# Performance work log

Hardware: AMD Instinct MI355X
Metric: run time of the kernel (lower is better)

## Reference

```python
import jax, jax.numpy as jnp
import numpy as np

B, CIN, COUT, K, SDIM, H, W = 16, 512, 512, 3, 512, 64, 64


def setup_inputs() -> dict:
    key = jax.random.key(0)
    k1, k2, k3, k4 = jax.random.split(key, 4)
    return {
        "x": jax.random.normal(k1, (B, CIN, H, W), dtype=jnp.float32),
        "style": jax.random.normal(k2, (B, SDIM), dtype=jnp.float32),
        "weight": jax.random.normal(k3, (COUT, CIN, K, K), dtype=jnp.float32),
        "style_w": jax.random.normal(k4, (CIN, SDIM), dtype=jnp.float32),
        "style_b": jnp.ones((CIN,), dtype=jnp.float32),  # bias.data.fill_(1.0)
    }


def reference(x, style, weight, style_w, style_b):
    batch, in_ch, h, w_size = x.shape
    out_ch, _, ks, _ = weight.shape
    pad = ks // 2
    # EqualizedLinear: runtime weight scaling by 1/sqrt(fan_in)
    lin_scale = 1.0 / np.sqrt(style_w.shape[1])
    s = style @ (style_w * lin_scale).T + style_b  # [B, Cin]
    # modulate
    conv_scale = 1.0 / np.sqrt(in_ch * ks * ks)
    wmod = (weight[None] * conv_scale) * s[:, None, :, None, None]  # [B,Cout,Cin,k,k]
    # demodulate
    dcoef = jax.lax.rsqrt(jnp.sum(jnp.square(wmod), axis=(2, 3, 4)) + 1e-8)  # [B,Cout]
    wmod = wmod * dcoef[:, :, None, None, None]
    # grouped conv with groups = batch
    x_r = x.reshape(1, batch * in_ch, h, w_size)
    w_r = wmod.reshape(batch * out_ch, in_ch, ks, ks)
    out = jax.lax.conv_general_dilated(
        x_r, w_r,
        window_strides=(1, 1),
        padding=[(pad, pad), (pad, pad)],
        dimension_numbers=("NCHW", "OIHW", "NCHW"),
        feature_group_count=batch,
    )
    return out.reshape(batch, out_ch, h, w_size)
```

## Files before the change

### kernel.cpp

```cpp
#include <hip/hip_runtime.h>
#include <math.h>

#define B 16
#define CIN 512
#define COUT 512
#define SDIM 512
#define H 64
#define W 64

typedef short s16x8 __attribute__((ext_vector_type(8)));
typedef float f32x4 __attribute__((ext_vector_type(4)));
typedef float f32x16 __attribute__((ext_vector_type(16)));

__device__ __constant__ float LIN_SCALE  = 0.04419417382415922f;
__device__ __constant__ float CONV_SCALE = 0.014731391274719742f;

__device__ __forceinline__ ushort f2bf(float f) {
  unsigned u = __float_as_uint(f);
  return (ushort)((u + 0x7FFFu + ((u >> 16) & 1u)) >> 16);
}

#define GLOAD16(g, l)                                           \
  __builtin_amdgcn_global_load_lds(                             \
      (const __attribute__((address_space(1))) unsigned*)(g),   \
      (__attribute__((address_space(3))) unsigned*)(l), 16, 0, 0)

__global__ __launch_bounds__(256) void prep1_kernel(
    const float* __restrict__ w, const float* __restrict__ style,
    const float* __restrict__ style_w, const float* __restrict__ style_b,
    ushort* __restrict__ wt, float* __restrict__ wsq, float* __restrict__ s,
    float* __restrict__ s2) {
  const int tid = threadIdx.x;
  if (blockIdx.x < 128) {
    const int t = blockIdx.x * 256 + tid;
    const int so = t & 3;
    const int chunk = (t >> 2) & 15;
    const int co = t >> 6;
    const float4* wp =
        (const float4*)(w + ((size_t)co * 512 + chunk * 32 + so * 8) * 9);
    float wv[72];
#pragma unroll
    for (int i = 0; i < 18; ++i) {
      float4 v = wp[i];
      wv[4 * i + 0] = v.x; wv[4 * i + 1] = v.y;
      wv[4 * i + 2] = v.z; wv[4 * i + 3] = v.w;
    }
    {
      float q[8];
#pragma unroll
      for (int i = 0; i < 8; ++i) {
        float a = 0.f;
#pragma unroll
        for (int k = 0; k < 9; ++k) {
          float v = wv[i * 9 + k];
          a += v * v;
        }
        q[i] = a;
      }
      float4* qd = (float4*)(wsq + (size_t)co * 512 + chunk * 32 + so * 8);
      qd[0] = make_float4(q[0], q[1], q[2], q[3]);
      qd[1] = make_float4(q[4], q[5], q[6], q[7]);
    }
    const int cb = co >> 6, co64 = co & 63;
    ushort* dst = wt + (size_t)chunk * 147456 + (size_t)cb * 2048 +
                  (size_t)so * 512 + (size_t)co64 * 8;
#pragma unroll
    for (int j = 0; j < 9; ++j) {
      s16x8 p;
#pragma unroll
      for (int i = 0; i < 8; ++i) p[i] = (short)f2bf(wv[i * 9 + j]);
      *(s16x8*)(dst + (size_t)j * 16384) = p;
    }
  } else {
    const int bb = blockIdx.x - 128;
    __shared__ float st[SDIM];
    st[tid] = style[bb * SDIM + tid];
    st[tid + 256] = style[bb * SDIM + tid + 256];
    __syncthreads();
#pragma unroll
    for (int half = 0; half < 2; ++half) {
      const int ci = tid + half * 256;
      const float4* wr =
          reinterpret_cast<const float4*>(style_w + (size_t)ci * SDIM);
      float acc = 0.f;
#pragma unroll 4
      for (int k = 0; k < SDIM / 4; ++k) {
        float4 wv = wr[k];
        acc += st[4 * k + 0] * wv.x + st[4 * k + 1] * wv.y +
               st[4 * k + 2] * wv.z + st[4 * k + 3] * wv.w;
      }
      float v = acc * LIN_SCALE + style_b[ci];
      s[bb * CIN + ci] = v;
      s2[bb * CIN + ci] = v * v;
    }
  }
}

__global__ __launch_bounds__(512) void dcoef_kernel(
    const float* __restrict__ s2, const float* __restrict__ wsq,
    float* __restrict__ outscale) {
  const int b = blockIdx.x;
  const int co = threadIdx.x;
  __shared__ float sh[CIN];
  sh[co] = s2[b * CIN + co];
  __syncthreads();

  const float4* wr = reinterpret_cast<const float4*>(wsq + (size_t)co * CIN);
  float acc = 0.f;
#pragma unroll 4
  for (int k = 0; k < CIN / 4; ++k) {
    float4 wv = wr[k];
    acc += sh[4 * k + 0] * wv.x + sh[4 * k + 1] * wv.y +
           sh[4 * k + 2] * wv.z + sh[4 * k + 3] * wv.w;
  }
  float d = rsqrtf(acc * CONV_SCALE * CONV_SCALE + 1e-8f);
  outscale[b * COUT + co] = d * CONV_SCALE;
}

__global__ __launch_bounds__(256) void pack_x_kernel(
    const float* __restrict__ x, const float* __restrict__ smod,
    ushort* __restrict__ xp) {
  __shared__ float xt[32][65];
  __shared__ float sm[32];
  const int tid = threadIdx.x;
  const int gr = blockIdx.x, chunk = blockIdx.y, b = blockIdx.z;
  if (tid < 32) sm[tid] = smod[b * 512 + chunk * 32 + tid];
  {
    const int ci = tid >> 3, cq = tid & 7;
    const float4* rp = (const float4*)(
        x + (((size_t)b * 512 + chunk * 32 + ci) * 64 + gr) * 64 + cq * 8);
    float4 a = rp[0], c2 = rp[1];
    float* row = &xt[ci][cq * 8];
    row[0] = a.x; row[1] = a.y; row[2] = a.z; row[3] = a.w;
    row[4] = c2.x; row[5] = c2.y; row[6] = c2.z; row[7] = c2.w;
  }
  __syncthreads();
  const int c = tid & 63, o = tid >> 6;
  s16x8 p;
#pragma unroll
  for (int i = 0; i < 8; ++i)
    p[i] = (short)f2bf(xt[o * 8 + i][c] * sm[o * 8 + i]);
  *(s16x8*)(xp + ((size_t)(b * 16 + chunk) * 64 + gr) * 2048 + o * 512 +
            c * 8) = p;
}

#define XSOFF8 36864
#define DLDS8 79104

__global__ __launch_bounds__(256, 2) void conv_mfma8_kernel(
    const ushort* __restrict__ wt, const ushort* __restrict__ xp,
    const float* __restrict__ outscale, float* __restrict__ out) {
  extern __shared__ char smem[];

  const int tid = threadIdx.x;
  const int hb = blockIdx.x;
  const int cb = blockIdx.y;
  const int b  = blockIdx.z;
  const int h0 = hb * 8, co0 = cb * 64;
  const int lane = tid & 63, wid = tid >> 6;
  const int l31 = lane & 31, hi = lane >> 5;

  {
    s16x8* p = (s16x8*)(smem + XSOFF8);
    for (int e = tid; e < 2640; e += 256) p[e] = (s16x8)0;
  }

  f32x16 acc[2][2][2];
#pragma unroll
  for (int rr = 0; rr < 2; ++rr)
#pragma unroll
    for (int mt = 0; mt < 2; ++mt)
#pragma unroll
      for (int nt = 0; nt < 2; ++nt) acc[rr][mt][nt] = (f32x16)0.f;

  int aoff[2][2];
#pragma unroll
  for (int mt = 0; mt < 2; ++mt)
#pragma unroll
    for (int ks = 0; ks < 2; ++ks)
      aoff[mt][ks] = (ks * 2 + hi) * 1024 + (mt * 32 + l31) * 16;
  int boff[3][2][2];
#pragma unroll
  for (int kw = 0; kw < 3; ++kw)
#pragma unroll
    for (int nt = 0; nt < 2; ++nt)
#pragma unroll
      for (int ks = 0; ks < 2; ++ks)
        boff[kw][nt][ks] =
            (ks * 2 + hi) * 1056 + (nt * 32 + l31 + kw) * 16;

  const char* wsrc0 = (const char*)wt + cb * 4096 + wid * 1024 + lane * 16;
  const char* xsrc0 =
      (const char*)xp + (size_t)b * 4194304 + wid * 1024 + lane * 16;
  char* wdst = smem + wid * 1024 + lane * 16;
  char* xdst = smem + XSOFF8 + wid * 1056 + 16 + lane * 16;
  const char* wb = smem;
  const char* xb = smem + XSOFF8 + 2 * wid * 4224;

  __syncthreads();

  for (int chunk = 0; chunk < 16; ++chunk) {
    const char* wsrc = wsrc0 + (size_t)chunk * 294912;
    const char* xsrc = xsrc0 + (size_t)chunk * 262144;
#pragma unroll
    for (int t = 0; t < 9; ++t)
      GLOAD16(wsrc + t * 32768, wdst + t * 4096);
#pragma unroll
    for (int t = 0; t < 10; ++t) {
      int gr = h0 - 1 + t;
      if ((unsigned)gr < 64u)
        GLOAD16(xsrc + (size_t)gr * 4096, xdst + t * 4224);
    }
    __syncthreads();

#pragma unroll
    for (int kw = 0; kw < 3; ++kw) {
      s16x8 bf[4][2][2];
#pragma unroll
      for (int q = 0; q < 4; ++q)
#pragma unroll
        for (int nt = 0; nt < 2; ++nt)
#pragma unroll
          for (int ks = 0; ks < 2; ++ks)
            bf[q][nt][ks] =
                *(const s16x8*)(xb + q * 4224 + boff[kw][nt][ks]);
#pragma unroll
      for (int kh = 0; kh < 3; ++kh) {
        const char* wj = wb + (kh * 3 + kw) * 4096;
#pragma unroll
        for (int ks = 0; ks < 2; ++ks) {
          s16x8 af0 = *(const s16x8*)(wj + aoff[0][ks]);
          s16x8 af1 = *(const s16x8*)(wj + aoff[1][ks]);
          __builtin_amdgcn_s_setprio(1);
#pragma unroll
          for (int rr = 0; rr < 2; ++rr)
#pragma unroll
            for (int nt = 0; nt < 2; ++nt) {
              acc[rr][0][nt] = __builtin_amdgcn_mfma_f32_32x32x16_bf16(
                  af0, bf[rr + kh][nt][ks], acc[rr][0][nt], 0, 0, 0);
              acc[rr][1][nt] = __builtin_amdgcn_mfma_f32_32x32x16_bf16(
                  af1, bf[rr + kh][nt][ks], acc[rr][1][nt], 0, 0, 0);
            }
          __builtin_amdgcn_s_setprio(0);
        }
      }
    }
    __syncthreads();
  }

#pragma unroll
  for (int mt = 0; mt < 2; ++mt) {
#pragma unroll
    for (int reg = 0; reg < 16; ++reg) {
      const int row = (reg & 3) + 8 * (reg >> 2) + 4 * hi;
      const int co = co0 + mt * 32 + row;
      const float osc = outscale[b * COUT + co];
      float* obase = out + ((size_t)b * COUT + co) * H * W;
#pragma unroll
      for (int rr = 0; rr < 2; ++rr) {
        const int h = h0 + 2 * wid + rr;
#pragma unroll
        for (int nt = 0; nt < 2; ++nt)
          obase[h * W + nt * 32 + l31] = acc[rr][mt][nt][reg] * osc;
      }
    }
  }
}

__global__ __launch_bounds__(256, 2) void conv_mfma_kernel(
    const float* __restrict__ x, const float* __restrict__ weight,
    const float* __restrict__ s, const float* __restrict__ outscale,
    float* __restrict__ out) {
  __shared__ ushort xs[6][66][32];
  __shared__ ushort ws[9][64][32];

  const int tid = threadIdx.x;
  const int hb = blockIdx.x;
  const int cb = blockIdx.y;
  const int b  = blockIdx.z;
  const int h0 = hb * 4;
  const int co0 = cb * 64;
  const int lane = tid & 63;
  const int wid = tid >> 6;
  const int l15 = lane & 15;
  const int l4  = lane >> 4;

  f32x4 acc[4][4];
#pragma unroll
  for (int mt = 0; mt < 4; ++mt)
#pragma unroll
    for (int nt = 0; nt < 4; ++nt) acc[mt][nt] = (f32x4)0.f;

  const int wq = tid & 3;
  const int wco = tid >> 2;

  for (int c0 = 0; c0 < CIN; c0 += 32) {
    {
      const float4* wp = reinterpret_cast<const float4*>(
          weight + ((size_t)(co0 + wco) * CIN + c0 + wq * 8) * 9);
      float wv[72];
#pragma unroll
      for (int t = 0; t < 18; ++t) {
        float4 v = wp[t];
        wv[4 * t + 0] = v.x; wv[4 * t + 1] = v.y;
        wv[4 * t + 2] = v.z; wv[4 * t + 3] = v.w;
      }
      float sv[8];
#pragma unroll
      for (int i = 0; i < 8; ++i) sv[i] = s[b * CIN + c0 + wq * 8 + i];
#pragma unroll
      for (int j = 0; j < 9; ++j) {
        s16x8 p;
#pragma unroll
        for (int i = 0; i < 8; ++i)
          p[i] = (short)f2bf(wv[i * 9 + j] * sv[i]);
        *reinterpret_cast<s16x8*>(&ws[j][wco][wq * 8]) = p;
      }
    }
#pragma unroll
    for (int it = 0; it < 7; ++it) {
      int e = tid + it * 256;
      if (e < 6 * 66 * 4) {
        int q = e & 3;
        int t2 = e >> 2;
        int cc = t2 % 66;
        int r = t2 / 66;
        int gr = h0 - 1 + r;
        int gc = cc - 1;
        s16x8 p;
        if ((unsigned)gr < H && (unsigned)gc < W) {
          const float* xp2 =
              x + (((size_t)b * CIN + c0 + q * 8) * H + gr) * W + gc;
#pragma unroll
          for (int i = 0; i < 8; ++i) p[i] = (short)f2bf(xp2[(size_t)i * H * W]);
        } else {
#pragma unroll
          for (int i = 0; i < 8; ++i) p[i] = 0;
        }
        *reinterpret_cast<s16x8*>(&xs[r][cc][q * 8]) = p;
      }
    }
    __syncthreads();

#pragma unroll
    for (int kh = 0; kh < 3; ++kh) {
#pragma unroll
      for (int kw = 0; kw < 3; ++kw) {
        const int j = kh * 3 + kw;
        s16x8 af[4], bf[4];
#pragma unroll
        for (int mt = 0; mt < 4; ++mt)
          af[mt] = *reinterpret_cast<const s16x8*>(
              &ws[j][mt * 16 + l15][l4 * 8]);
#pragma unroll
        for (int nt = 0; nt < 4; ++nt)
          bf[nt] = *reinterpret_cast<const s16x8*>(
              &xs[wid + kh][nt * 16 + l15 + kw][l4 * 8]);
#pragma unroll
        for (int mt = 0; mt < 4; ++mt)
#pragma unroll
          for (int nt = 0; nt < 4; ++nt)
            acc[mt][nt] = __builtin_amdgcn_mfma_f32_16x16x32_bf16(
                af[mt], bf[nt], acc[mt][nt], 0, 0, 0);
      }
    }
    __syncthreads();
  }

  const int h = h0 + wid;
#pragma unroll
  for (int mt = 0; mt < 4; ++mt) {
#pragma unroll
    for (int r = 0; r < 4; ++r) {
      const int co = co0 + mt * 16 + l4 * 4 + r;
      const float osc = outscale[b * COUT + co];
      float* orow = out + (((size_t)b * COUT + co) * H + h) * W;
#pragma unroll
      for (int nt = 0; nt < 4; ++nt)
        orow[nt * 16 + l15] = acc[mt][nt][r] * osc;
    }
  }
}

extern "C" void kernel_launch(void* const* d_in, const int* in_sizes, int n_in,
                              void* d_out, int out_size, void* d_ws,
                              size_t ws_size, hipStream_t stream) {
  const float* x = (const float*)d_in[0];
  const float* style = (const float*)d_in[1];
  const float* weight = (const float*)d_in[2];
  const float* style_w = (const float*)d_in[3];
  const float* style_b = (const float*)d_in[4];
  float* out = (float*)d_out;

  char* wsb = (char*)d_ws;
  float* s = (float*)(wsb + 0);
  float* s2 = (float*)(wsb + 32768);
  float* wsq = (float*)(wsb + 65536);
  float* outscale = (float*)(wsb + 1114112);
  ushort* wt = (ushort*)(wsb + 1146880);
  ushort* xp = (ushort*)(wsb + 5865472);
  const size_t NEED = 72974336;

  hipError_t attr_ok = hipFuncSetAttribute(
      reinterpret_cast<const void*>(conv_mfma8_kernel),
      hipFuncAttributeMaxDynamicSharedMemorySize, DLDS8);

  if (attr_ok == hipSuccess && ws_size >= NEED) {
    prep1_kernel<<<144, 256, 0, stream>>>(weight, style, style_w, style_b, wt,
                                          wsq, s, s2);
    dcoef_kernel<<<B, 512, 0, stream>>>(s2, wsq, outscale);
    pack_x_kernel<<<dim3(64, 16, 16), 256, 0, stream>>>(x, s, xp);
    conv_mfma8_kernel<<<dim3(8, 8, 16), 256, DLDS8, stream>>>(wt, xp, outscale,
                                                              out);
  } else {
    prep1_kernel<<<144, 256, 0, stream>>>(weight, style, style_w, style_b, wt,
                                          wsq, s, s2);
    dcoef_kernel<<<B, 512, 0, stream>>>(s2, wsq, outscale);
    conv_mfma_kernel<<<dim3(16, 8, 16), 256, 0, stream>>>(x, weight, s,
                                                          outscale, out);
  }
}
```

Measured before the change: 352.4 us.

## Double-buffer conv LDS stages with 16-channel chunks and repacked layouts

The conv kernel now splits the input channels into 32 chunks of 16 instead of 16 chunks of 32, and keeps two LDS buffers of the same total size. The next chunk is loaded with global_load_lds while the current one is computed, so one barrier per iteration replaces the two-barrier load-then-compute loop. The weight and x packing kernels are changed to write the matching chunk-contiguous layouts so each stage is one contiguous copy. The per-chunk MFMA work halves and the setprio hints are dropped, which adds loop and sync overhead per unit of math. The single barrier before compute may not wait for the async LDS loads (no explicit vmcnt wait shown), which is a correctness and timing risk.

```diff
diff --git a/kernel.cpp b/kernel.cpp
--- a/kernel.cpp
+++ b/kernel.cpp
@@ -33,11 +33,11 @@
   const int tid = threadIdx.x;
   if (blockIdx.x < 128) {
     const int t = blockIdx.x * 256 + tid;
-    const int so = t & 3;
-    const int chunk = (t >> 2) & 15;
+    const int so = t & 1;
+    const int chunk = (t >> 1) & 31;
     const int co = t >> 6;
-    const float4* wp =
-        (const float4*)(w + ((size_t)co * 512 + chunk * 32 + so * 8) * 9);
+    const float4* wp = (const float4*)(
+        w + ((size_t)co * 512 + chunk * 16 + so * 8) * 9);
     float wv[72];
 #pragma unroll
     for (int i = 0; i < 18; ++i) {
@@ -57,19 +57,19 @@
         }
         q[i] = a;
       }
-      float4* qd = (float4*)(wsq + (size_t)co * 512 + chunk * 32 + so * 8);
+      float4* qd = (float4*)(wsq + (size_t)co * 512 + chunk * 16 + so * 8);
       qd[0] = make_float4(q[0], q[1], q[2], q[3]);
       qd[1] = make_float4(q[4], q[5], q[6], q[7]);
     }
     const int cb = co >> 6, co64 = co & 63;
-    ushort* dst = wt + (size_t)chunk * 147456 + (size_t)cb * 2048 +
+    ushort* dst = wt + (size_t)chunk * 73728 + (size_t)cb * 9216 +
                   (size_t)so * 512 + (size_t)co64 * 8;
 #pragma unroll
     for (int j = 0; j < 9; ++j) {
       s16x8 p;
 #pragma unroll
       for (int i = 0; i < 8; ++i) p[i] = (short)f2bf(wv[i * 9 + j]);
-      *(s16x8*)(dst + (size_t)j * 16384) = p;
+      *(s16x8*)(dst + (size_t)j * 1024) = p;
     }
   } else {
     const int bb = blockIdx.x - 128;
@@ -123,12 +123,12 @@
   __shared__ float xt[32][65];
   __shared__ float sm[32];
   const int tid = threadIdx.x;
-  const int gr = blockIdx.x, chunk = blockIdx.y, b = blockIdx.z;
-  if (tid < 32) sm[tid] = smod[b * 512 + chunk * 32 + tid];
+  const int gr = blockIdx.x, cp = blockIdx.y, b = blockIdx.z;
+  if (tid < 32) sm[tid] = smod[b * 512 + cp * 32 + tid];
   {
     const int ci = tid >> 3, cq = tid & 7;
     const float4* rp = (const float4*)(
-        x + (((size_t)b * 512 + chunk * 32 + ci) * 64 + gr) * 64 + cq * 8);
+        x + (((size_t)b * 512 + cp * 32 + ci) * 64 + gr) * 64 + cq * 8);
     float4 a = rp[0], c2 = rp[1];
     float* row = &xt[ci][cq * 8];
     row[0] = a.x; row[1] = a.y; row[2] = a.z; row[3] = a.w;
@@ -140,14 +140,17 @@
 #pragma unroll
   for (int i = 0; i < 8; ++i)
     p[i] = (short)f2bf(xt[o * 8 + i][c] * sm[o * 8 + i]);
-  *(s16x8*)(xp + ((size_t)(b * 16 + chunk) * 64 + gr) * 2048 + o * 512 +
-            c * 8) = p;
-}
-
-#define XSOFF8 36864
-#define DLDS8 79104
-
-__global__ __launch_bounds__(256, 2) void conv_mfma8_kernel(
+  const int chunk = cp * 2 + (o >> 1), oct = o & 1;
+  *(s16x8*)(xp + (size_t)b * 2097152 + (size_t)chunk * 65536 + oct * 32768 +
+            gr * 512 + c * 8) = p;
+}
+
+#define CBUF_WS 18432
+#define CBUF_XS 21120
+#define XS_BASE 36864
+#define DLDS9 79104
+
+__global__ __launch_bounds__(256, 2) void conv_mfma9_kernel(
     const ushort* __restrict__ wt, const ushort* __restrict__ xp,
     const float* __restrict__ outscale, float* __restrict__ out) {
   extern __shared__ char smem[];
@@ -161,7 +164,7 @@
   const int l31 = lane & 31, hi = lane >> 5;
 
   {
-    s16x8* p = (s16x8*)(smem + XSOFF8);
+    s16x8* p = (s16x8*)(smem + XS_BASE);
     for (int e = tid; e < 2640; e += 256) p[e] = (s16x8)0;
   }
 
@@ -173,79 +176,79 @@
 #pragma unroll
       for (int nt = 0; nt < 2; ++nt) acc[rr][mt][nt] = (f32x16)0.f;
 
-  int aoff[2][2];
+  int aoff[2];
 #pragma unroll
   for (int mt = 0; mt < 2; ++mt)
-#pragma unroll
-    for (int ks = 0; ks < 2; ++ks)
-      aoff[mt][ks] = (ks * 2 + hi) * 1024 + (mt * 32 + l31) * 16;
-  int boff[3][2][2];
+    aoff[mt] = hi * 1024 + (mt * 32 + l31) * 16;
+  int boff[3][2];
 #pragma unroll
   for (int kw = 0; kw < 3; ++kw)
 #pragma unroll
     for (int nt = 0; nt < 2; ++nt)
-#pragma unroll
-      for (int ks = 0; ks < 2; ++ks)
-        boff[kw][nt][ks] =
-            (ks * 2 + hi) * 1056 + (nt * 32 + l31 + kw) * 16;
-
-  const char* wsrc0 = (const char*)wt + cb * 4096 + wid * 1024 + lane * 16;
-  const char* xsrc0 =
-      (const char*)xp + (size_t)b * 4194304 + wid * 1024 + lane * 16;
-  char* wdst = smem + wid * 1024 + lane * 16;
-  char* xdst = smem + XSOFF8 + wid * 1056 + 16 + lane * 16;
-  const char* wb = smem;
-  const char* xb = smem + XSOFF8 + 2 * wid * 4224;
+      boff[kw][nt] = hi * 10560 + (nt * 32 + l31 + kw) * 16;
+
+  const char* wsrc0 = (const char*)wt + (size_t)cb * 18432;
+  const char* xsrc0 = (const char*)xp + (size_t)b * 4194304;
+
+  auto stage = [&](int chunk, int buf) {
+    const char* wsrc = wsrc0 + (size_t)chunk * 147456;
+    const char* xsrc = xsrc0 + (size_t)chunk * 131072;
+    char* wd = smem + buf * CBUF_WS;
+    char* xd = smem + XS_BASE + buf * CBUF_XS;
+#pragma unroll
+    for (int p = 0; p < 4; ++p)
+      GLOAD16(wsrc + p * 4096 + tid * 16, wd + p * 4096 + tid * 16);
+    if (tid < 128)
+      GLOAD16(wsrc + 16384 + tid * 16, wd + 16384 + tid * 16);
+#pragma unroll
+    for (int p = 0; p < 5; ++p) {
+      int e = p * 4 + wid;
+      int oct = (e >= 10) ? 1 : 0;
+      int r = e - oct * 10;
+      int gr = h0 - 1 + r;
+      if ((unsigned)gr < 64u)
+        GLOAD16(xsrc + oct * 65536 + gr * 1024 + lane * 16,
+                xd + oct * 10560 + r * 1056 + 16 + lane * 16);
+    }
+  };
+
+  auto compute = [&](int buf) {
+    const char* wb2 = smem + buf * CBUF_WS;
+    const char* xb2 = smem + XS_BASE + buf * CBUF_XS + 2 * wid * 1056;
+#pragma unroll
+    for (int kw = 0; kw < 3; ++kw) {
+      s16x8 bf[4][2];
+#pragma unroll
+      for (int q = 0; q < 4; ++q)
+#pragma unroll
+        for (int nt = 0; nt < 2; ++nt)
+          bf[q][nt] = *(const s16x8*)(xb2 + q * 1056 + boff[kw][nt]);
+#pragma unroll
+      for (int kh = 0; kh < 3; ++kh) {
+        const char* wj = wb2 + (kh * 3 + kw) * 2048;
+        s16x8 af0 = *(const s16x8*)(wj + aoff[0]);
+        s16x8 af1 = *(const s16x8*)(wj + aoff[1]);
+#pragma unroll
+        for (int rr = 0; rr < 2; ++rr)
+#pragma unroll
+          for (int nt = 0; nt < 2; ++nt) {
+            acc[rr][0][nt] = __builtin_amdgcn_mfma_f32_32x32x16_bf16(
+                af0, bf[rr + kh][nt], acc[rr][0][nt], 0, 0, 0);
+            acc[rr][1][nt] = __builtin_amdgcn_mfma_f32_32x32x16_bf16(
+                af1, bf[rr + kh][nt], acc[rr][1][nt], 0, 0, 0);
+          }
+      }
+    }
+  };
 
   __syncthreads();
-
-  for (int chunk = 0; chunk < 16; ++chunk) {
-    const char* wsrc = wsrc0 + (size_t)chunk * 294912;
-    const char* xsrc = xsrc0 + (size_t)chunk * 262144;
-#pragma unroll
-    for (int t = 0; t < 9; ++t)
-      GLOAD16(wsrc + t * 32768, wdst + t * 4096);
-#pragma unroll
-    for (int t = 0; t < 10; ++t) {
-      int gr = h0 - 1 + t;
-      if ((unsigned)gr < 64u)
-        GLOAD16(xsrc + (size_t)gr * 4096, xdst + t * 4224);
-    }
+  stage(0, 0);
+
+  for (int c = 0; c < 32; ++c) {
+    const int buf = c & 1;
     __syncthreads();
-
-#pragma unroll
-    for (int kw = 0; kw < 3; ++kw) {
-      s16x8 bf[4][2][2];
-#pragma unroll
-      for (int q = 0; q < 4; ++q)
-#pragma unroll
-        for (int nt = 0; nt < 2; ++nt)
-#pragma unroll
-          for (int ks = 0; ks < 2; ++ks)
-            bf[q][nt][ks] =
-                *(const s16x8*)(xb + q * 4224 + boff[kw][nt][ks]);
-#pragma unroll
-      for (int kh = 0; kh < 3; ++kh) {
-        const char* wj = wb + (kh * 3 + kw) * 4096;
-#pragma unroll
-        for (int ks = 0; ks < 2; ++ks) {
-          s16x8 af0 = *(const s16x8*)(wj + aoff[0][ks]);
-          s16x8 af1 = *(const s16x8*)(wj + aoff[1][ks]);
-          __builtin_amdgcn_s_setprio(1);
-#pragma unroll
-          for (int rr = 0; rr < 2; ++rr)
-#pragma unroll
-            for (int nt = 0; nt < 2; ++nt) {
-              acc[rr][0][nt] = __builtin_amdgcn_mfma_f32_32x32x16_bf16(
-                  af0, bf[rr + kh][nt][ks], acc[rr][0][nt], 0, 0, 0);
-              acc[rr][1][nt] = __builtin_amdgcn_mfma_f32_32x32x16_bf16(
-                  af1, bf[rr + kh][nt][ks], acc[rr][1][nt], 0, 0, 0);
-            }
-          __builtin_amdgcn_s_setprio(0);
-        }
-      }
-    }
-    __syncthreads();
+    if (c + 1 < 32) stage(c + 1, buf ^ 1);
+    compute(buf);
   }
 
 #pragma unroll
@@ -402,15 +405,15 @@
   const size_t NEED = 72974336;
 
   hipError_t attr_ok = hipFuncSetAttribute(
-      reinterpret_cast<const void*>(conv_mfma8_kernel),
-      hipFuncAttributeMaxDynamicSharedMemorySize, DLDS8);
+      reinterpret_cast<const void*>(conv_mfma9_kernel),
+      hipFuncAttributeMaxDynamicSharedMemorySize, DLDS9);
 
   if (attr_ok == hipSuccess && ws_size >= NEED) {
     prep1_kernel<<<144, 256, 0, stream>>>(weight, style, style_w, style_b, wt,
                                           wsq, s, s2);
     dcoef_kernel<<<B, 512, 0, stream>>>(s2, wsq, outscale);
     pack_x_kernel<<<dim3(64, 16, 16), 256, 0, stream>>>(x, s, xp);
-    conv_mfma8_kernel<<<dim3(8, 8, 16), 256, DLDS8, stream>>>(wt, xp, outscale,
+    conv_mfma9_kernel<<<dim3(8, 8, 16), 256, DLDS9, stream>>>(wt, xp, outscale,
                                                               out);
   } else {
     prep1_kernel<<<144, 256, 0, stream>>>(weight, style, style_w, style_b, wt,
```

New measurement: 334.4 us. -5.1%, faster.
